# Kernel optimization log

Hardware: AMD Instinct MI355X
Metric: run time of the kernel (lower is better)

Reference implementation:

```python
import jax, jax.numpy as jnp
import numpy as np

NEG_INF = -1e10
DIST_THRESH = 0


def _collect_entities(rep, pos, mask):
    # rep: [B, N, H]; pos: [B, M, S] int; mask: [B, M, S] float
    B, M, S = pos.shape
    g = jnp.take_along_axis(rep, pos.reshape(B, M * S)[:, :, None], axis=1)  # [B, M*S, H]
    g = g.reshape(B, M, S, rep.shape[-1]) * mask[..., None]
    return g.sum(axis=2)  # [B, M, H]


def setup_inputs() -> dict:
    key = jax.random.key(0)
    ks = jax.random.split(key, 10)
    B, N, H = 8, 2048, 512
    M, S = 96, 16
    E, D, R, MAXD = 256, 64, 5, 600
    scale = 0.02
    return {
        'node_hidden': jax.random.normal(ks[0], (B, N, H), jnp.float32),
        'chem_map': jax.random.randint(ks[1], (B, M, S), 0, N),
        'chem_mask': jnp.ones((B, M, S), jnp.float32),
        'dis_map': jax.random.randint(ks[2], (B, M, S), 0, N),
        'dis_mask': jnp.ones((B, M, S), jnp.float32),
        'distance': jax.random.randint(ks[3], (B, M, M), 0, MAXD),
        'W_chem': jax.random.normal(ks[4], (H, E), jnp.float32) * scale,
        'b_chem': jnp.zeros((E,), jnp.float32),
        'W_dis': jax.random.normal(ks[5], (H, E), jnp.float32) * scale,
        'b_dis': jnp.zeros((E,), jnp.float32),
        'W_score': jax.random.normal(ks[6], (2 * E + H + D, R), jnp.float32) * scale,
        'b_score': jnp.zeros((R,), jnp.float32),
        'dist_emb': jax.random.normal(ks[7], (MAXD, D), jnp.float32) * scale,
    }


def reference(node_hidden, chem_map, chem_mask, dis_map, dis_mask, distance,
              W_chem, b_chem, W_dis, b_dis, W_score, b_score, dist_emb):
    B, M = chem_map.shape[0], chem_map.shape[1]
    E = W_chem.shape[1]

    # sentence representation: max-pool over tokens  -> [B, H]
    sent = jnp.max(node_hidden, axis=1)

    # gather mention spans, masked sum pool, tanh-linear  -> [B, M, E]
    chem = jnp.tanh(_collect_entities(node_hidden, chem_map, chem_mask) @ W_chem + b_chem)
    dis = jnp.tanh(_collect_entities(node_hidden, dis_map, dis_mask) @ W_dis + b_dis)

    dist_e = dist_emb[distance]  # [B, M, M, D]

    # pairwise concat: [chem_i, dis_j, dist_ij, sent]  -> [B, M, M, 2E+D+H]
    concat = jnp.concatenate([
        jnp.broadcast_to(chem[:, :, None, :], (B, M, M, E)),
        jnp.broadcast_to(dis[:, None, :, :], (B, M, M, E)),
        dist_e,
        jnp.broadcast_to(sent[:, None, None, :], (B, M, M, sent.shape[-1])),
    ], axis=-1)

    score = jnp.einsum('bmnf,fr->bmnr', concat, W_score) + b_score  # [B, M, M, R]

    # validity masks: non-empty spans and distance >= threshold
    chem_valid = chem_mask.sum(axis=-1) > 0  # [B, M]
    dis_valid = dis_mask.sum(axis=-1) > 0    # [B, M]
    pair_valid = chem_valid[:, :, None] & dis_valid[:, None, :]  # [B, M, M]
    valid = pair_valid & (distance >= DIST_THRESH)
    score = jnp.where(valid[..., None], score, NEG_INF)

    # max-pool over all mention pairs  -> [B, R]
    return jnp.max(score.reshape(B, M * M, -1), axis=1)
```

## Files before the change

### kernel.cpp

```cpp
#include <hip/hip_runtime.h>
#include <math.h>

constexpr int B = 8, N = 2048, H = 512, M = 96, S = 16;
constexpr int E = 256, D = 64, R = 5, MAXD = 600;
constexpr int NZ = 64;
constexpr int NCHUNK = N / NZ;
constexpr int MT = 8;
constexpr int HC = 4;
constexpr int HCHUNK = H / HC;
constexpr float NEG_INF = -1e10f;

constexpr int K1_SENT = 256;
constexpr int K1_POOL = 2 * B * M;
constexpr int K2_GEMM = (M / MT) * B * 2 * HC;
constexpr int K2_SENT = B;
constexpr int K2_DIST = MAXD / 4;

__device__ inline void atomicMaxFloat(float* addr, float val) {
    int* ai = (int*)addr;
    int old = *ai;
    while (__int_as_float(old) < val) {
        int assumed = old;
        old = atomicCAS(ai, assumed, __float_as_int(val));
        if (old == assumed) break;
    }
}

__global__ void k1(const float* __restrict__ node,
                   const int* __restrict__ cmap, const float* __restrict__ cmask,
                   const int* __restrict__ dmap, const float* __restrict__ dmask,
                   float* __restrict__ part, float* __restrict__ pooled,
                   float* __restrict__ validAB) {
    int blk = blockIdx.x, t = threadIdx.x;
    __shared__ int   smap[S];
    __shared__ float smask[S];

    if (blk < K1_SENT) {
        int b = blk >> 5;
        int z = ((blk & 31) << 1) + (t >> 7);
        int tt = t & 127;
        const float4* p = reinterpret_cast<const float4*>(
            node + ((size_t)b * N + (size_t)z * NCHUNK) * H) + tt;
        float4 mx = p[0];
        #pragma unroll
        for (int n = 1; n < NCHUNK; ++n) {
            float4 v = p[(size_t)n * (H / 4)];
            mx.x = fmaxf(mx.x, v.x); mx.y = fmaxf(mx.y, v.y);
            mx.z = fmaxf(mx.z, v.z); mx.w = fmaxf(mx.w, v.w);
        }
        reinterpret_cast<float4*>(part + ((size_t)z * B + b) * H)[tt] = mx;
    } else {
        int j = blk - K1_SENT;
        int m = j % M, b = (j / M) % B, z = j / (M * B);
        const int*   map  = z ? dmap  : cmap;
        const float* mask = z ? dmask : cmask;
        if (t < S) {
            size_t off = ((size_t)b * M + m) * S + t;
            smap[t]  = map[off];
            smask[t] = mask[off];
        }
        __syncthreads();
        float a0 = 0.f, a1 = 0.f;
        #pragma unroll
        for (int s = 0; s < S; ++s) {
            float mk = smask[s];
            const float2 v = reinterpret_cast<const float2*>(
                node + ((size_t)b * N + smap[s]) * H)[t];
            a0 += mk * v.x; a1 += mk * v.y;
        }
        size_t row = ((size_t)z * B + b) * M + m;
        reinterpret_cast<float2*>(pooled + row * H)[t] = make_float2(a0, a1);
        if (t == 0) {
            float ms = 0.f;
            #pragma unroll
            for (int s = 0; s < S; ++s) ms += smask[s];
            validAB[row] = (ms > 0.f) ? 1.f : 0.f;
        }
    }
}

__global__ void k2(const float* __restrict__ pooled,
                   const float* __restrict__ Wc, const float* __restrict__ Wd,
                   const float* __restrict__ part, const float* __restrict__ Wsc,
                   const float* __restrict__ bsc, const float* __restrict__ emb,
                   float* __restrict__ dotp, float* __restrict__ sS,
                   float* __restrict__ sD, float* __restrict__ out) {
    int blk = blockIdx.x, t = threadIdx.x;
    __shared__ float lp[MT][HCHUNK];
    __shared__ float sent[H];
    __shared__ float red[R][4];

    if (blk < K2_GEMM) {
        int mg  = blk % (M / MT);
        int b   = (blk / (M / MT)) % B;
        int zhc = blk / ((M / MT) * B);
        int z = zhc >> 2, hc = zhc & 3;
        const float* W = z ? Wd : Wc;

        for (int i = t; i < MT * HCHUNK; i += 256) {
            int mi = i >> 7, hh = i & (HCHUNK - 1);
            lp[mi][hh] = pooled[(((size_t)z * B + b) * M + mg * MT + mi) * H + hc * HCHUNK + hh];
        }
        __syncthreads();

        float acc[MT] = {};
        const float* Wp = W + (size_t)(hc * HCHUNK) * E + t;
        for (int hh = 0; hh < HCHUNK; hh += 4) {
            float w0 = Wp[(size_t)(hh + 0) * E];
            float w1 = Wp[(size_t)(hh + 1) * E];
            float w2 = Wp[(size_t)(hh + 2) * E];
            float w3 = Wp[(size_t)(hh + 3) * E];
            #pragma unroll
            for (int mi = 0; mi < MT; ++mi) {
                const float4 pv = *reinterpret_cast<const float4*>(&lp[mi][hh]);
                acc[mi] += pv.x * w0 + pv.y * w1 + pv.z * w2 + pv.w * w3;
            }
        }
        #pragma unroll
        for (int mi = 0; mi < MT; ++mi) {
            size_t row = ((size_t)z * B + b) * M + mg * MT + mi;
            dotp[((size_t)hc * (2 * B * M) + row) * E + t] = acc[mi];
        }
    } else if (blk < K2_GEMM + K2_SENT) {
        int b = blk - K2_GEMM;
        if (b == 0 && t < B * R) out[t] = NEG_INF;
        for (int h = t; h < H; h += 256) {
            float mx = -INFINITY;
            for (int z = 0; z < NZ; ++z) mx = fmaxf(mx, part[((size_t)z * B + b) * H + h]);
            sent[h] = mx;
        }
        __syncthreads();
        float acc[R] = {};
        for (int h = t; h < H; h += 256) {
            float v = sent[h];
            const float* w = Wsc + (size_t)(2 * E + D + h) * R;
            #pragma unroll
            for (int r = 0; r < R; ++r) acc[r] += v * w[r];
        }
        int wave = t >> 6, lane = t & 63;
        #pragma unroll
        for (int r = 0; r < R; ++r) {
            float v = acc[r];
            for (int off = 32; off; off >>= 1) v += __shfl_down(v, off, 64);
            if (lane == 0) red[r][wave] = v;
        }
        __syncthreads();
        if (t < R) sS[b * R + t] = red[t][0] + red[t][1] + red[t][2] + red[t][3] + bsc[t];
    } else {
        int d = (blk - K2_GEMM - K2_SENT) * 4 + (t >> 6);
        int k = t & 63;
        float v = emb[(size_t)d * D + k];
        #pragma unroll
        for (int r = 0; r < R; ++r) {
            float p = v * Wsc[(size_t)(2 * E + k) * R + r];
            for (int off = 32; off; off >>= 1) p += __shfl_down(p, off, 64);
            if (k == 0) sD[d * R + r] = p;
        }
    }
}

__global__ void k3(const float* __restrict__ dotp,
                   const float* __restrict__ bc, const float* __restrict__ bd,
                   const float* __restrict__ Wsc, const float* __restrict__ sS,
                   float* __restrict__ sAB) {
    int rid = blockIdx.x * 4 + (threadIdx.x >> 6);
    int lane = threadIdx.x & 63;
    int z = rid / (B * M);
    int b = (rid % (B * M)) / M;
    const float* bias = z ? bd : bc;
    int scoff = z ? E : 0;

    float4 dv = make_float4(0.f, 0.f, 0.f, 0.f);
    #pragma unroll
    for (int hc = 0; hc < HC; ++hc) {
        float4 v = reinterpret_cast<const float4*>(dotp + ((size_t)hc * (2 * B * M) + rid) * E)[lane];
        dv.x += v.x; dv.y += v.y; dv.z += v.z; dv.w += v.w;
    }
    float4 bv = reinterpret_cast<const float4*>(bias)[lane];
    float v0 = tanhf(dv.x + bv.x);
    float v1 = tanhf(dv.y + bv.y);
    float v2 = tanhf(dv.z + bv.z);
    float v3 = tanhf(dv.w + bv.w);

    int e0 = scoff + lane * 4;
    float p[R];
    #pragma unroll
    for (int r = 0; r < R; ++r) {
        p[r] = v0 * Wsc[(size_t)(e0 + 0) * R + r] + v1 * Wsc[(size_t)(e0 + 1) * R + r]
             + v2 * Wsc[(size_t)(e0 + 2) * R + r] + v3 * Wsc[(size_t)(e0 + 3) * R + r];
    }
    #pragma unroll
    for (int r = 0; r < R; ++r) {
        for (int off = 32; off; off >>= 1) p[r] += __shfl_down(p[r], off, 64);
    }
    if (lane == 0) {
        #pragma unroll
        for (int r = 0; r < R; ++r) {
            float add = (z == 0) ? sS[b * R + r] : 0.f;
            sAB[(size_t)rid * R + r] = p[r] + add;
        }
    }
}

__global__ void k4(const int* __restrict__ distance,
                   const float* __restrict__ sAB, const float* __restrict__ validAB,
                   const float* __restrict__ sD, float* __restrict__ out) {
    int g = blockIdx.x, b = blockIdx.y;
    int t = threadIdx.x;
    __shared__ float lB[M * R];
    __shared__ float lD[MAXD * R];
    __shared__ float lA[MT * R];
    __shared__ float lvA[MT], lvB[M];
    __shared__ float red[R][4];

    for (int i = t; i < M * R; i += 256) lB[i] = sAB[((size_t)(B + b)) * M * R + i];
    for (int i = t; i < MAXD * R; i += 256) lD[i] = sD[i];
    if (t < MT * R) lA[t] = sAB[((size_t)b * M + g * MT) * R + t];
    if (t < MT) lvA[t] = validAB[(size_t)b * M + g * MT + t];
    for (int i = t; i < M; i += 256) lvB[i] = validAB[((size_t)B + b) * M + i];
    __syncthreads();

    float mx[R];
    #pragma unroll
    for (int r = 0; r < R; ++r) mx[r] = NEG_INF;

    #pragma unroll
    for (int it = 0; it < (MT * M) / 256; ++it) {
        int idx = it * 256 + t;
        int mi = idx / M, n = idx % M;
        int dist = distance[((size_t)b * M + g * MT + mi) * M + n];
        if (lvA[mi] > 0.f && lvB[n] > 0.f && dist >= 0 ) {
            #pragma unroll
            for (int r = 0; r < R; ++r)
                mx[r] = fmaxf(mx[r], lA[mi * R + r] + lB[n * R + r] + lD[dist * R + r]);
        }
    }
    int wave = t >> 6, lane = t & 63;
    #pragma unroll
    for (int r = 0; r < R; ++r) {
        float v = mx[r];
        for (int off = 32; off; off >>= 1) v = fmaxf(v, __shfl_down(v, off, 64));
        if (lane == 0) red[r][wave] = v;
    }
    __syncthreads();
    if (t < R) {
        float v = fmaxf(fmaxf(red[t][0], red[t][1]), fmaxf(red[t][2], red[t][3]));
        atomicMaxFloat(out + b * R + t, v);
    }
}

extern "C" void kernel_launch(void* const* d_in, const int* in_sizes, int n_in,
                              void* d_out, int out_size, void* d_ws, size_t ws_size,
                              hipStream_t stream) {
    const float* node     = (const float*)d_in[0];
    const int*   cmap     = (const int*)  d_in[1];
    const float* cmask    = (const float*)d_in[2];
    const int*   dmap     = (const int*)  d_in[3];
    const float* dmask    = (const float*)d_in[4];
    const int*   distance = (const int*)  d_in[5];
    const float* Wc       = (const float*)d_in[6];
    const float* bc       = (const float*)d_in[7];
    const float* Wd       = (const float*)d_in[8];
    const float* bd       = (const float*)d_in[9];
    const float* Wsc      = (const float*)d_in[10];
    const float* bsc      = (const float*)d_in[11];
    const float* emb      = (const float*)d_in[12];
    float* out = (float*)d_out;

    float* ws      = (float*)d_ws;
    float* part    = ws;
    float* sS      = part + (size_t)NZ * B * H;
    float* sAB     = sS + B * R;
    float* validAB = sAB + 2 * B * M * R;
    float* sD      = validAB + 2 * B * M;
    float* pooled  = sD + MAXD * R;
    float* dotp    = pooled + (size_t)2 * B * M * H;

    hipLaunchKernelGGL(k1, dim3(K1_SENT + K1_POOL), dim3(256), 0, stream,
                       node, cmap, cmask, dmap, dmask, part, pooled, validAB);
    hipLaunchKernelGGL(k2, dim3(K2_GEMM + K2_SENT + K2_DIST), dim3(256), 0, stream,
                       pooled, Wc, Wd, part, Wsc, bsc, emb, dotp, sS, sD, out);
    hipLaunchKernelGGL(k3, dim3(2 * B * M / 4), dim3(256), 0, stream,
                       dotp, bc, bd, Wsc, sS, sAB);
    hipLaunchKernelGGL(k4, dim3(M / MT, B), dim3(256), 0, stream,
                       distance, sAB, validAB, sD, out);
}
```

Measured before the change: 61.34 us.

## Fuse four kernels into one cooperative persistent kernel with grid syncs

Replaces the four-launch pipeline with a single cooperative kernel that runs three phases separated by grid.sync. The GEMM stage now covers the full hidden dimension per block and fuses bias, tanh and the score projection in place, which removes the dotp partials and the separate k3 pass. The aim is to cut launch gaps and intermediate global traffic. In exchange it adds grid-wide barrier cost, and fewer GEMM blocks each do longer serial work. The old multi-kernel path is kept as a fallback if the cooperative launch fails.

```diff
diff --git a/kernel.cpp b/kernel.cpp
--- a/kernel.cpp
+++ b/kernel.cpp
@@ -1,20 +1,25 @@
 #include <hip/hip_runtime.h>
+#include <hip/hip_cooperative_groups.h>
 #include <math.h>
+
+namespace cg = cooperative_groups;
 
 constexpr int B = 8, N = 2048, H = 512, M = 96, S = 16;
 constexpr int E = 256, D = 64, R = 5, MAXD = 600;
 constexpr int NZ = 64;
 constexpr int NCHUNK = N / NZ;
-constexpr int MT = 8;
+constexpr int MT2 = 4;
+constexpr int MT  = 8;
 constexpr int HC = 4;
 constexpr int HCHUNK = H / HC;
+constexpr int MT4 = 8;
 constexpr float NEG_INF = -1e10f;
 
-constexpr int K1_SENT = 256;
-constexpr int K1_POOL = 2 * B * M;
-constexpr int K2_GEMM = (M / MT) * B * 2 * HC;
-constexpr int K2_SENT = B;
-constexpr int K2_DIST = MAXD / 4;
+constexpr int P1_SENT  = 256;
+constexpr int P1_ITEMS = P1_SENT + 2 * B * M;
+constexpr int NGEMM    = (M / MT2) * B * 2;
+constexpr int P2_ITEMS = NGEMM + B + MAXD / 4;
+constexpr int P3_ITEMS = (M / MT4) * B;
 
 __device__ inline void atomicMaxFloat(float* addr, float val) {
     int* ai = (int*)addr;
@@ -25,6 +30,225 @@
         if (old == assumed) break;
     }
 }
+
+__global__ __launch_bounds__(256, 4)
+void k_all(const float* __restrict__ node,
+           const int* __restrict__ cmap, const float* __restrict__ cmask,
+           const int* __restrict__ dmap, const float* __restrict__ dmask,
+           const int* __restrict__ distance,
+           const float* __restrict__ Wc, const float* __restrict__ bc,
+           const float* __restrict__ Wd, const float* __restrict__ bd,
+           const float* __restrict__ Wsc, const float* __restrict__ bsc,
+           const float* __restrict__ emb,
+           float* __restrict__ part, float* __restrict__ pooled,
+           float* __restrict__ validAB, float* __restrict__ sS,
+           float* __restrict__ sAB, float* __restrict__ sD,
+           float* __restrict__ out) {
+    cg::grid_group grid = cg::this_grid();
+    const int t = threadIdx.x;
+    const int blk = blockIdx.x;
+    const int GD = gridDim.x;
+
+    __shared__ float4 lp4[MT2][H / 4];
+    __shared__ int    smap[S];
+    __shared__ float  smask[S];
+    __shared__ float  sent[H];
+    __shared__ float  red2[4][MT2 * R];
+    __shared__ float  red[R][4];
+    __shared__ float  lB[M * R];
+    __shared__ float  lD[MAXD * R];
+    __shared__ float  lA[MT4 * R];
+    __shared__ float  lvA[MT4], lvB[M];
+
+    for (int item = blk; item < P1_ITEMS; item += GD) {
+        if (item < P1_SENT) {
+            int b = item >> 5;
+            int z = ((item & 31) << 1) + (t >> 7);
+            int tt = t & 127;
+            const float4* p = reinterpret_cast<const float4*>(
+                node + ((size_t)b * N + (size_t)z * NCHUNK) * H) + tt;
+            float4 mx = p[0];
+            #pragma unroll
+            for (int n = 1; n < NCHUNK; ++n) {
+                float4 v = p[(size_t)n * (H / 4)];
+                mx.x = fmaxf(mx.x, v.x); mx.y = fmaxf(mx.y, v.y);
+                mx.z = fmaxf(mx.z, v.z); mx.w = fmaxf(mx.w, v.w);
+            }
+            reinterpret_cast<float4*>(part + ((size_t)z * B + b) * H)[tt] = mx;
+        } else {
+            int j = item - P1_SENT;
+            int m = j % M, b = (j / M) % B, z = j / (M * B);
+            const int*   map  = z ? dmap  : cmap;
+            const float* mask = z ? dmask : cmask;
+            __syncthreads();
+            if (t < S) {
+                size_t off = ((size_t)b * M + m) * S + t;
+                smap[t]  = map[off];
+                smask[t] = mask[off];
+            }
+            __syncthreads();
+            float a0 = 0.f, a1 = 0.f;
+            #pragma unroll
+            for (int s = 0; s < S; ++s) {
+                float mk = smask[s];
+                const float2 v = reinterpret_cast<const float2*>(
+                    node + ((size_t)b * N + smap[s]) * H)[t];
+                a0 += mk * v.x; a1 += mk * v.y;
+            }
+            size_t row = ((size_t)z * B + b) * M + m;
+            reinterpret_cast<float2*>(pooled + row * H)[t] = make_float2(a0, a1);
+            if (t == 0) {
+                float ms = 0.f;
+                #pragma unroll
+                for (int s = 0; s < S; ++s) ms += smask[s];
+                validAB[row] = (ms > 0.f) ? 1.f : 0.f;
+            }
+        }
+    }
+    if (blk == 0 && t < B * R) out[t] = NEG_INF;
+
+    grid.sync();
+
+    for (int item = blk; item < P2_ITEMS; item += GD) {
+        __syncthreads();
+        if (item < NGEMM) {
+            int mg = item % (M / MT2);
+            int b  = (item / (M / MT2)) % B;
+            int z  = item / ((M / MT2) * B);
+            const float* W    = z ? Wd : Wc;
+            const float* bias = z ? bd : bc;
+            int scoff = z ? E : 0;
+
+            for (int i = t; i < MT2 * (H / 4); i += 256) {
+                int mi = i >> 7, c4 = i & 127;
+                lp4[mi][c4] = reinterpret_cast<const float4*>(
+                    pooled + (((size_t)z * B + b) * M + mg * MT2 + mi) * H)[c4];
+            }
+            __syncthreads();
+
+            float acc[MT2] = {};
+            const float* Wp = W + t;
+            for (int h = 0; h < H; h += 4) {
+                float w0 = Wp[(size_t)(h + 0) * E];
+                float w1 = Wp[(size_t)(h + 1) * E];
+                float w2 = Wp[(size_t)(h + 2) * E];
+                float w3 = Wp[(size_t)(h + 3) * E];
+                #pragma unroll
+                for (int mi = 0; mi < MT2; ++mi) {
+                    const float4 pv = lp4[mi][h >> 2];
+                    acc[mi] += pv.x * w0 + pv.y * w1 + pv.z * w2 + pv.w * w3;
+                }
+            }
+            float be = bias[t];
+            float v[MT2];
+            #pragma unroll
+            for (int mi = 0; mi < MT2; ++mi) v[mi] = tanhf(acc[mi] + be);
+
+            float w5[R];
+            #pragma unroll
+            for (int r = 0; r < R; ++r) w5[r] = Wsc[(size_t)(scoff + t) * R + r];
+            int wave = t >> 6, lane = t & 63;
+            #pragma unroll
+            for (int mi = 0; mi < MT2; ++mi) {
+                #pragma unroll
+                for (int r = 0; r < R; ++r) {
+                    float p = v[mi] * w5[r];
+                    for (int off = 32; off; off >>= 1) p += __shfl_down(p, off, 64);
+                    if (lane == 0) red2[wave][mi * R + r] = p;
+                }
+            }
+            __syncthreads();
+            if (t < MT2 * R) {
+                float s = red2[0][t] + red2[1][t] + red2[2][t] + red2[3][t];
+                int mi = t / R, r = t % R;
+                sAB[(((size_t)z * B + b) * M + mg * MT2 + mi) * R + r] = s;
+            }
+        } else if (item < NGEMM + B) {
+            int b = item - NGEMM;
+            for (int h = t; h < H; h += 256) {
+                float mx = -INFINITY;
+                for (int z = 0; z < NZ; ++z) mx = fmaxf(mx, part[((size_t)z * B + b) * H + h]);
+                sent[h] = mx;
+            }
+            __syncthreads();
+            float acc[R] = {};
+            for (int h = t; h < H; h += 256) {
+                float v = sent[h];
+                const float* w = Wsc + (size_t)(2 * E + D + h) * R;
+                #pragma unroll
+                for (int r = 0; r < R; ++r) acc[r] += v * w[r];
+            }
+            int wave = t >> 6, lane = t & 63;
+            #pragma unroll
+            for (int r = 0; r < R; ++r) {
+                float v = acc[r];
+                for (int off = 32; off; off >>= 1) v += __shfl_down(v, off, 64);
+                if (lane == 0) red[r][wave] = v;
+            }
+            __syncthreads();
+            if (t < R) sS[b * R + t] = red[t][0] + red[t][1] + red[t][2] + red[t][3] + bsc[t];
+        } else {
+            int d = (item - NGEMM - B) * 4 + (t >> 6);
+            int k = t & 63;
+            float v = emb[(size_t)d * D + k];
+            #pragma unroll
+            for (int r = 0; r < R; ++r) {
+                float p = v * Wsc[(size_t)(2 * E + k) * R + r];
+                for (int off = 32; off; off >>= 1) p += __shfl_down(p, off, 64);
+                if (k == 0) sD[d * R + r] = p;
+            }
+        }
+    }
+
+    grid.sync();
+
+    for (int item = blk; item < P3_ITEMS; item += GD) {
+        int g = item % (M / MT4);
+        int b = item / (M / MT4);
+        __syncthreads();
+
+        for (int i = t; i < M * R; i += 256) lB[i] = sAB[((size_t)(B + b)) * M * R + i];
+        for (int i = t; i < MAXD * R; i += 256) lD[i] = sD[i];
+        if (t < MT4 * R) lA[t] = sAB[((size_t)b * M + g * MT4) * R + t] + sS[b * R + (t % R)];
+        if (t < MT4) lvA[t] = validAB[(size_t)b * M + g * MT4 + t];
+        for (int i = t; i < M; i += 256) lvB[i] = validAB[((size_t)B + b) * M + i];
+        __syncthreads();
+
+        float mx[R];
+        #pragma unroll
+        for (int r = 0; r < R; ++r) mx[r] = NEG_INF;
+
+        #pragma unroll
+        for (int it = 0; it < (MT4 * M) / 256; ++it) {
+            int idx = it * 256 + t;
+            int mi = idx / M, n = idx % M;
+            int dist = distance[((size_t)b * M + g * MT4 + mi) * M + n];
+            if (lvA[mi] > 0.f && lvB[n] > 0.f && dist >= 0 ) {
+                #pragma unroll
+                for (int r = 0; r < R; ++r)
+                    mx[r] = fmaxf(mx[r], lA[mi * R + r] + lB[n * R + r] + lD[dist * R + r]);
+            }
+        }
+        int wave = t >> 6, lane = t & 63;
+        #pragma unroll
+        for (int r = 0; r < R; ++r) {
+            float v = mx[r];
+            for (int off = 32; off; off >>= 1) v = fmaxf(v, __shfl_down(v, off, 64));
+            if (lane == 0) red[r][wave] = v;
+        }
+        __syncthreads();
+        if (t < R) {
+            float v = fmaxf(fmaxf(red[t][0], red[t][1]), fmaxf(red[t][2], red[t][3]));
+            atomicMaxFloat(out + b * R + t, v);
+        }
+    }
+}
+
+constexpr int K1_SENT = 256;
+constexpr int K1_POOL = 2 * B * M;
+constexpr int K2_GEMM = (M / MT) * B * 2 * HC;
+constexpr int K2_SENT = B;
+constexpr int K2_DIST = MAXD / 4;
 
 __global__ void k1(const float* __restrict__ node,
                    const int* __restrict__ cmap, const float* __restrict__ cmask,
@@ -34,7 +258,6 @@
     int blk = blockIdx.x, t = threadIdx.x;
     __shared__ int   smap[S];
     __shared__ float smask[S];
-
     if (blk < K1_SENT) {
         int b = blk >> 5;
         int z = ((blk & 31) << 1) + (t >> 7);
@@ -89,20 +312,17 @@
     __shared__ float lp[MT][HCHUNK];
     __shared__ float sent[H];
     __shared__ float red[R][4];
-
     if (blk < K2_GEMM) {
         int mg  = blk % (M / MT);
         int b   = (blk / (M / MT)) % B;
         int zhc = blk / ((M / MT) * B);
         int z = zhc >> 2, hc = zhc & 3;
         const float* W = z ? Wd : Wc;
-
         for (int i = t; i < MT * HCHUNK; i += 256) {
             int mi = i >> 7, hh = i & (HCHUNK - 1);
             lp[mi][hh] = pooled[(((size_t)z * B + b) * M + mg * MT + mi) * H + hc * HCHUNK + hh];
         }
         __syncthreads();
-
         float acc[MT] = {};
         const float* Wp = W + (size_t)(hc * HCHUNK) * E + t;
         for (int hh = 0; hh < HCHUNK; hh += 4) {
@@ -169,7 +389,6 @@
     int b = (rid % (B * M)) / M;
     const float* bias = z ? bd : bc;
     int scoff = z ? E : 0;
-
     float4 dv = make_float4(0.f, 0.f, 0.f, 0.f);
     #pragma unroll
     for (int hc = 0; hc < HC; ++hc) {
@@ -181,7 +400,6 @@
     float v1 = tanhf(dv.y + bv.y);
     float v2 = tanhf(dv.z + bv.z);
     float v3 = tanhf(dv.w + bv.w);
-
     int e0 = scoff + lane * 4;
     float p[R];
     #pragma unroll
@@ -209,27 +427,24 @@
     int t = threadIdx.x;
     __shared__ float lB[M * R];
     __shared__ float lD[MAXD * R];
-    __shared__ float lA[MT * R];
-    __shared__ float lvA[MT], lvB[M];
+    __shared__ float lA[MT4 * R];
+    __shared__ float lvA[MT4], lvB[M];
     __shared__ float red[R][4];
-
     for (int i = t; i < M * R; i += 256) lB[i] = sAB[((size_t)(B + b)) * M * R + i];
     for (int i = t; i < MAXD * R; i += 256) lD[i] = sD[i];
-    if (t < MT * R) lA[t] = sAB[((size_t)b * M + g * MT) * R + t];
-    if (t < MT) lvA[t] = validAB[(size_t)b * M + g * MT + t];
+    if (t < MT4 * R) lA[t] = sAB[((size_t)b * M + g * MT4) * R + t];
+    if (t < MT4) lvA[t] = validAB[(size_t)b * M + g * MT4 + t];
     for (int i = t; i < M; i += 256) lvB[i] = validAB[((size_t)B + b) * M + i];
     __syncthreads();
-
     float mx[R];
     #pragma unroll
     for (int r = 0; r < R; ++r) mx[r] = NEG_INF;
-
     #pragma unroll
-    for (int it = 0; it < (MT * M) / 256; ++it) {
+    for (int it = 0; it < (MT4 * M) / 256; ++it) {
         int idx = it * 256 + t;
         int mi = idx / M, n = idx % M;
-        int dist = distance[((size_t)b * M + g * MT + mi) * M + n];
-        if (lvA[mi] > 0.f && lvB[n] > 0.f && dist >= 0 ) {
+        int dist = distance[((size_t)b * M + g * MT4 + mi) * M + n];
+        if (lvA[mi] > 0.f && lvB[n] > 0.f && dist >= 0) {
             #pragma unroll
             for (int r = 0; r < R; ++r)
                 mx[r] = fmaxf(mx[r], lA[mi * R + r] + lB[n * R + r] + lD[dist * R + r]);
@@ -276,12 +491,30 @@
     float* pooled  = sD + MAXD * R;
     float* dotp    = pooled + (size_t)2 * B * M * H;
 
-    hipLaunchKernelGGL(k1, dim3(K1_SENT + K1_POOL), dim3(256), 0, stream,
-                       node, cmap, cmask, dmap, dmask, part, pooled, validAB);
-    hipLaunchKernelGGL(k2, dim3(K2_GEMM + K2_SENT + K2_DIST), dim3(256), 0, stream,
-                       pooled, Wc, Wd, part, Wsc, bsc, emb, dotp, sS, sD, out);
-    hipLaunchKernelGGL(k3, dim3(2 * B * M / 4), dim3(256), 0, stream,
-                       dotp, bc, bd, Wsc, sS, sAB);
-    hipLaunchKernelGGL(k4, dim3(M / MT, B), dim3(256), 0, stream,
-                       distance, sAB, validAB, sD, out);
-}
+    int occ = 0;
+    hipError_t qerr = hipOccupancyMaxActiveBlocksPerMultiprocessor(&occ, k_all, 256, 0);
+    int grid = occ * 256;
+    if (grid > 1024) grid = 1024;
+
+    hipError_t lerr = hipErrorUnknown;
+    if (qerr == hipSuccess && grid >= 64) {
+        void* args[] = {
+            (void*)&node, (void*)&cmap, (void*)&cmask, (void*)&dmap, (void*)&dmask,
+            (void*)&distance, (void*)&Wc, (void*)&bc, (void*)&Wd, (void*)&bd,
+            (void*)&Wsc, (void*)&bsc, (void*)&emb,
+            (void*)&part, (void*)&pooled, (void*)&validAB, (void*)&sS,
+            (void*)&sAB, (void*)&sD, (void*)&out
+        };
+        lerr = hipLaunchCooperativeKernel((void*)k_all, dim3(grid), dim3(256), args, 0, stream);
+    }
+    if (lerr != hipSuccess) {
+        hipLaunchKernelGGL(k1, dim3(K1_SENT + K1_POOL), dim3(256), 0, stream,
+                           node, cmap, cmask, dmap, dmask, part, pooled, validAB);
+        hipLaunchKernelGGL(k2, dim3(K2_GEMM + K2_SENT + K2_DIST), dim3(256), 0, stream,
+                           pooled, Wc, Wd, part, Wsc, bsc, emb, dotp, sS, sD, out);
+        hipLaunchKernelGGL(k3, dim3(2 * B * M / 4), dim3(256), 0, stream,
+                           dotp, bc, bd, Wsc, sS, sAB);
+        hipLaunchKernelGGL(k4, dim3(M / MT4, B), dim3(256), 0, stream,
+                           distance, sAB, validAB, sD, out);
+    }
+}
```

New measurement: 183.4 us. 199% more time.

## Fuse four kernels into two, computing span pooling and projection in one block

Applied to the files above, without the earlier changes.

Merges the gather-pool, projection GEMM, tanh and score-reduction stages into one kernel in which each block pools four mentions into shared memory and immediately multiplies them by the full H×E weight. The per-batch sentence score is moved into the final max kernel. This removes two launches and the global round trips through the pooled and split-K dotp buffers. In exchange, each GEMM block now walks the full H=512 reduction serially with only 4 rows per weight load, so weight reuse drops. Every final block also recomputes the sentence max over 64 partials.

```diff
diff --git a/kernel.cpp b/kernel.cpp
--- a/kernel.cpp
+++ b/kernel.cpp
@@ -5,16 +5,14 @@
 constexpr int E = 256, D = 64, R = 5, MAXD = 600;
 constexpr int NZ = 64;
 constexpr int NCHUNK = N / NZ;
-constexpr int MT = 8;
-constexpr int HC = 4;
-constexpr int HCHUNK = H / HC;
+constexpr int MTA = 4;
+constexpr int MT4 = 8;
 constexpr float NEG_INF = -1e10f;
 
-constexpr int K1_SENT = 256;
-constexpr int K1_POOL = 2 * B * M;
-constexpr int K2_GEMM = (M / MT) * B * 2 * HC;
-constexpr int K2_SENT = B;
-constexpr int K2_DIST = MAXD / 4;
+constexpr int A_SENT = 256;
+constexpr int A_GEMM = 2 * B * (M / MTA);
+constexpr int A_DIST = MAXD / 4;
+constexpr int A_GRID = A_SENT + A_GEMM + A_DIST;
 
 __device__ inline void atomicMaxFloat(float* addr, float val) {
     int* ai = (int*)addr;
@@ -26,16 +24,21 @@
     }
 }
 
-__global__ void k1(const float* __restrict__ node,
+__global__ void kA(const float* __restrict__ node,
                    const int* __restrict__ cmap, const float* __restrict__ cmask,
                    const int* __restrict__ dmap, const float* __restrict__ dmask,
-                   float* __restrict__ part, float* __restrict__ pooled,
-                   float* __restrict__ validAB) {
-    int blk = blockIdx.x, t = threadIdx.x;
-    __shared__ int   smap[S];
-    __shared__ float smask[S];
-
-    if (blk < K1_SENT) {
+                   const float* __restrict__ Wc, const float* __restrict__ bc,
+                   const float* __restrict__ Wd, const float* __restrict__ bd,
+                   const float* __restrict__ Wsc, const float* __restrict__ emb,
+                   float* __restrict__ part, float* __restrict__ sAB,
+                   float* __restrict__ validAB, float* __restrict__ sD,
+                   float* __restrict__ out) {
+    const int blk = blockIdx.x;
+    const int t = threadIdx.x;
+
+    if (blk == 0 && t < B * R) out[t] = NEG_INF;
+
+    if (blk < A_SENT) {
         int b = blk >> 5;
         int z = ((blk & 31) << 1) + (t >> 7);
         int tt = t & 127;
@@ -49,105 +52,85 @@
             mx.z = fmaxf(mx.z, v.z); mx.w = fmaxf(mx.w, v.w);
         }
         reinterpret_cast<float4*>(part + ((size_t)z * B + b) * H)[tt] = mx;
-    } else {
-        int j = blk - K1_SENT;
-        int m = j % M, b = (j / M) % B, z = j / (M * B);
+    } else if (blk < A_SENT + A_GEMM) {
+        int j  = blk - A_SENT;
+        int mg = j % (M / MTA);
+        int b  = (j / (M / MTA)) % B;
+        int z  = j / ((M / MTA) * B);
+        const float* W    = z ? Wd : Wc;
+        const float* bias = z ? bd : bc;
         const int*   map  = z ? dmap  : cmap;
         const float* mask = z ? dmask : cmask;
-        if (t < S) {
-            size_t off = ((size_t)b * M + m) * S + t;
-            smap[t]  = map[off];
-            smask[t] = mask[off];
+        int scoff = z ? E : 0;
+
+        __shared__ float pooled[MTA][H];
+        __shared__ int   smap[MTA][S];
+        __shared__ float smask[MTA][S];
+
+        if (t < MTA * S) {
+            int mi = t >> 4, s = t & 15;
+            size_t off = ((size_t)b * M + mg * MTA + mi) * S + s;
+            smap[mi][s]  = map[off];
+            smask[mi][s] = mask[off];
         }
         __syncthreads();
-        float a0 = 0.f, a1 = 0.f;
-        #pragma unroll
-        for (int s = 0; s < S; ++s) {
-            float mk = smask[s];
-            const float2 v = reinterpret_cast<const float2*>(
-                node + ((size_t)b * N + smap[s]) * H)[t];
-            a0 += mk * v.x; a1 += mk * v.y;
-        }
-        size_t row = ((size_t)z * B + b) * M + m;
-        reinterpret_cast<float2*>(pooled + row * H)[t] = make_float2(a0, a1);
-        if (t == 0) {
+
+        #pragma unroll
+        for (int mi = 0; mi < MTA; ++mi) {
+            float a0 = 0.f, a1 = 0.f;
+            #pragma unroll
+            for (int s = 0; s < S; ++s) {
+                float mk = smask[mi][s];
+                const float2 v = reinterpret_cast<const float2*>(
+                    node + ((size_t)b * N + smap[mi][s]) * H)[t];
+                a0 += mk * v.x; a1 += mk * v.y;
+            }
+            reinterpret_cast<float2*>(&pooled[mi][0])[t] = make_float2(a0, a1);
+        }
+        if (t < MTA) {
             float ms = 0.f;
             #pragma unroll
-            for (int s = 0; s < S; ++s) ms += smask[s];
-            validAB[row] = (ms > 0.f) ? 1.f : 0.f;
-        }
-    }
-}
-
-__global__ void k2(const float* __restrict__ pooled,
-                   const float* __restrict__ Wc, const float* __restrict__ Wd,
-                   const float* __restrict__ part, const float* __restrict__ Wsc,
-                   const float* __restrict__ bsc, const float* __restrict__ emb,
-                   float* __restrict__ dotp, float* __restrict__ sS,
-                   float* __restrict__ sD, float* __restrict__ out) {
-    int blk = blockIdx.x, t = threadIdx.x;
-    __shared__ float lp[MT][HCHUNK];
-    __shared__ float sent[H];
-    __shared__ float red[R][4];
-
-    if (blk < K2_GEMM) {
-        int mg  = blk % (M / MT);
-        int b   = (blk / (M / MT)) % B;
-        int zhc = blk / ((M / MT) * B);
-        int z = zhc >> 2, hc = zhc & 3;
-        const float* W = z ? Wd : Wc;
-
-        for (int i = t; i < MT * HCHUNK; i += 256) {
-            int mi = i >> 7, hh = i & (HCHUNK - 1);
-            lp[mi][hh] = pooled[(((size_t)z * B + b) * M + mg * MT + mi) * H + hc * HCHUNK + hh];
+            for (int s = 0; s < S; ++s) ms += smask[t][s];
+            validAB[((size_t)z * B + b) * M + mg * MTA + t] = (ms > 0.f) ? 1.f : 0.f;
         }
         __syncthreads();
 
-        float acc[MT] = {};
-        const float* Wp = W + (size_t)(hc * HCHUNK) * E + t;
-        for (int hh = 0; hh < HCHUNK; hh += 4) {
-            float w0 = Wp[(size_t)(hh + 0) * E];
-            float w1 = Wp[(size_t)(hh + 1) * E];
-            float w2 = Wp[(size_t)(hh + 2) * E];
-            float w3 = Wp[(size_t)(hh + 3) * E];
-            #pragma unroll
-            for (int mi = 0; mi < MT; ++mi) {
-                const float4 pv = *reinterpret_cast<const float4*>(&lp[mi][hh]);
-                acc[mi] += pv.x * w0 + pv.y * w1 + pv.z * w2 + pv.w * w3;
-            }
-        }
-        #pragma unroll
-        for (int mi = 0; mi < MT; ++mi) {
-            size_t row = ((size_t)z * B + b) * M + mg * MT + mi;
-            dotp[((size_t)hc * (2 * B * M) + row) * E + t] = acc[mi];
-        }
-    } else if (blk < K2_GEMM + K2_SENT) {
-        int b = blk - K2_GEMM;
-        if (b == 0 && t < B * R) out[t] = NEG_INF;
-        for (int h = t; h < H; h += 256) {
-            float mx = -INFINITY;
-            for (int z = 0; z < NZ; ++z) mx = fmaxf(mx, part[((size_t)z * B + b) * H + h]);
-            sent[h] = mx;
-        }
-        __syncthreads();
-        float acc[R] = {};
-        for (int h = t; h < H; h += 256) {
-            float v = sent[h];
-            const float* w = Wsc + (size_t)(2 * E + D + h) * R;
-            #pragma unroll
-            for (int r = 0; r < R; ++r) acc[r] += v * w[r];
-        }
-        int wave = t >> 6, lane = t & 63;
+        int eq = t & 63;
+        int mi = t >> 6;
+        const float4* W4 = reinterpret_cast<const float4*>(W) + eq;
+        const float* pm = &pooled[mi][0];
+        float4 acc = make_float4(0.f, 0.f, 0.f, 0.f);
+        #pragma unroll 8
+        for (int h = 0; h < H; ++h) {
+            float4 wv = W4[(size_t)h * (E / 4)];
+            float p = pm[h];
+            acc.x += p * wv.x; acc.y += p * wv.y;
+            acc.z += p * wv.z; acc.w += p * wv.w;
+        }
+        float4 bv = reinterpret_cast<const float4*>(bias)[eq];
+        float v0 = tanhf(acc.x + bv.x);
+        float v1 = tanhf(acc.y + bv.y);
+        float v2 = tanhf(acc.z + bv.z);
+        float v3 = tanhf(acc.w + bv.w);
+
+        int e0 = scoff + 4 * eq;
+        float p[R];
         #pragma unroll
         for (int r = 0; r < R; ++r) {
-            float v = acc[r];
-            for (int off = 32; off; off >>= 1) v += __shfl_down(v, off, 64);
-            if (lane == 0) red[r][wave] = v;
-        }
-        __syncthreads();
-        if (t < R) sS[b * R + t] = red[t][0] + red[t][1] + red[t][2] + red[t][3] + bsc[t];
+            p[r] = v0 * Wsc[(size_t)(e0 + 0) * R + r] + v1 * Wsc[(size_t)(e0 + 1) * R + r]
+                 + v2 * Wsc[(size_t)(e0 + 2) * R + r] + v3 * Wsc[(size_t)(e0 + 3) * R + r];
+        }
+        #pragma unroll
+        for (int r = 0; r < R; ++r) {
+            for (int off = 32; off; off >>= 1) p[r] += __shfl_down(p[r], off, 64);
+        }
+        if (eq == 0) {
+            size_t row = ((size_t)z * B + b) * M + mg * MTA + mi;
+            #pragma unroll
+            for (int r = 0; r < R; ++r) sAB[row * R + r] = p[r];
+        }
     } else {
-        int d = (blk - K2_GEMM - K2_SENT) * 4 + (t >> 6);
+        int d = (blk - A_SENT - A_GEMM) * 4 + (t >> 6);
         int k = t & 63;
         float v = emb[(size_t)d * D + k];
         #pragma unroll
@@ -159,64 +142,53 @@
     }
 }
 
-__global__ void k3(const float* __restrict__ dotp,
-                   const float* __restrict__ bc, const float* __restrict__ bd,
-                   const float* __restrict__ Wsc, const float* __restrict__ sS,
-                   float* __restrict__ sAB) {
-    int rid = blockIdx.x * 4 + (threadIdx.x >> 6);
-    int lane = threadIdx.x & 63;
-    int z = rid / (B * M);
-    int b = (rid % (B * M)) / M;
-    const float* bias = z ? bd : bc;
-    int scoff = z ? E : 0;
-
-    float4 dv = make_float4(0.f, 0.f, 0.f, 0.f);
-    #pragma unroll
-    for (int hc = 0; hc < HC; ++hc) {
-        float4 v = reinterpret_cast<const float4*>(dotp + ((size_t)hc * (2 * B * M) + rid) * E)[lane];
-        dv.x += v.x; dv.y += v.y; dv.z += v.z; dv.w += v.w;
-    }
-    float4 bv = reinterpret_cast<const float4*>(bias)[lane];
-    float v0 = tanhf(dv.x + bv.x);
-    float v1 = tanhf(dv.y + bv.y);
-    float v2 = tanhf(dv.z + bv.z);
-    float v3 = tanhf(dv.w + bv.w);
-
-    int e0 = scoff + lane * 4;
-    float p[R];
-    #pragma unroll
-    for (int r = 0; r < R; ++r) {
-        p[r] = v0 * Wsc[(size_t)(e0 + 0) * R + r] + v1 * Wsc[(size_t)(e0 + 1) * R + r]
-             + v2 * Wsc[(size_t)(e0 + 2) * R + r] + v3 * Wsc[(size_t)(e0 + 3) * R + r];
-    }
-    #pragma unroll
-    for (int r = 0; r < R; ++r) {
-        for (int off = 32; off; off >>= 1) p[r] += __shfl_down(p[r], off, 64);
-    }
-    if (lane == 0) {
-        #pragma unroll
-        for (int r = 0; r < R; ++r) {
-            float add = (z == 0) ? sS[b * R + r] : 0.f;
-            sAB[(size_t)rid * R + r] = p[r] + add;
-        }
-    }
-}
-
-__global__ void k4(const int* __restrict__ distance,
+__global__ void kB(const float* __restrict__ part, const float* __restrict__ Wsc,
+                   const float* __restrict__ bsc,
+                   const int* __restrict__ distance,
                    const float* __restrict__ sAB, const float* __restrict__ validAB,
                    const float* __restrict__ sD, float* __restrict__ out) {
-    int g = blockIdx.x, b = blockIdx.y;
-    int t = threadIdx.x;
+    const int g = blockIdx.x % (M / MT4);
+    const int b = blockIdx.x / (M / MT4);
+    const int t = threadIdx.x;
+
+    __shared__ float sent[H];
+    __shared__ float red[R][4];
+    __shared__ float sSb[R];
     __shared__ float lB[M * R];
     __shared__ float lD[MAXD * R];
-    __shared__ float lA[MT * R];
-    __shared__ float lvA[MT], lvB[M];
-    __shared__ float red[R][4];
+    __shared__ float lA[MT4 * R];
+    __shared__ float lvA[MT4], lvB[M];
+
+    for (int h = t; h < H; h += 256) {
+        float mx = -INFINITY;
+        #pragma unroll 8
+        for (int z = 0; z < NZ; ++z) mx = fmaxf(mx, part[((size_t)z * B + b) * H + h]);
+        sent[h] = mx;
+    }
+    __syncthreads();
+
+    float acc[R] = {};
+    for (int h = t; h < H; h += 256) {
+        float v = sent[h];
+        const float* w = Wsc + (size_t)(2 * E + D + h) * R;
+        #pragma unroll
+        for (int r = 0; r < R; ++r) acc[r] += v * w[r];
+    }
+    int wave = t >> 6, lane = t & 63;
+    #pragma unroll
+    for (int r = 0; r < R; ++r) {
+        float v = acc[r];
+        for (int off = 32; off; off >>= 1) v += __shfl_down(v, off, 64);
+        if (lane == 0) red[r][wave] = v;
+    }
+    __syncthreads();
+    if (t < R) sSb[t] = red[t][0] + red[t][1] + red[t][2] + red[t][3] + bsc[t];
+    __syncthreads();
 
     for (int i = t; i < M * R; i += 256) lB[i] = sAB[((size_t)(B + b)) * M * R + i];
     for (int i = t; i < MAXD * R; i += 256) lD[i] = sD[i];
-    if (t < MT * R) lA[t] = sAB[((size_t)b * M + g * MT) * R + t];
-    if (t < MT) lvA[t] = validAB[(size_t)b * M + g * MT + t];
+    if (t < MT4 * R) lA[t] = sAB[((size_t)b * M + g * MT4) * R + t] + sSb[t % R];
+    if (t < MT4) lvA[t] = validAB[(size_t)b * M + g * MT4 + t];
     for (int i = t; i < M; i += 256) lvB[i] = validAB[((size_t)B + b) * M + i];
     __syncthreads();
 
@@ -225,17 +197,16 @@
     for (int r = 0; r < R; ++r) mx[r] = NEG_INF;
 
     #pragma unroll
-    for (int it = 0; it < (MT * M) / 256; ++it) {
+    for (int it = 0; it < (MT4 * M) / 256; ++it) {
         int idx = it * 256 + t;
         int mi = idx / M, n = idx % M;
-        int dist = distance[((size_t)b * M + g * MT + mi) * M + n];
+        int dist = distance[((size_t)b * M + g * MT4 + mi) * M + n];
         if (lvA[mi] > 0.f && lvB[n] > 0.f && dist >= 0 ) {
             #pragma unroll
             for (int r = 0; r < R; ++r)
                 mx[r] = fmaxf(mx[r], lA[mi * R + r] + lB[n * R + r] + lD[dist * R + r]);
         }
     }
-    int wave = t >> 6, lane = t & 63;
     #pragma unroll
     for (int r = 0; r < R; ++r) {
         float v = mx[r];
@@ -269,19 +240,13 @@
 
     float* ws      = (float*)d_ws;
     float* part    = ws;
-    float* sS      = part + (size_t)NZ * B * H;
-    float* sAB     = sS + B * R;
+    float* sAB     = part + (size_t)NZ * B * H;
     float* validAB = sAB + 2 * B * M * R;
     float* sD      = validAB + 2 * B * M;
-    float* pooled  = sD + MAXD * R;
-    float* dotp    = pooled + (size_t)2 * B * M * H;
-
-    hipLaunchKernelGGL(k1, dim3(K1_SENT + K1_POOL), dim3(256), 0, stream,
-                       node, cmap, cmask, dmap, dmask, part, pooled, validAB);
-    hipLaunchKernelGGL(k2, dim3(K2_GEMM + K2_SENT + K2_DIST), dim3(256), 0, stream,
-                       pooled, Wc, Wd, part, Wsc, bsc, emb, dotp, sS, sD, out);
-    hipLaunchKernelGGL(k3, dim3(2 * B * M / 4), dim3(256), 0, stream,
-                       dotp, bc, bd, Wsc, sS, sAB);
-    hipLaunchKernelGGL(k4, dim3(M / MT, B), dim3(256), 0, stream,
-                       distance, sAB, validAB, sD, out);
-}
+
+    hipLaunchKernelGGL(kA, dim3(A_GRID), dim3(256), 0, stream,
+                       node, cmap, cmask, dmap, dmask, Wc, bc, Wd, bd, Wsc, emb,
+                       part, sAB, validAB, sD, out);
+    hipLaunchKernelGGL(kB, dim3((M / MT4) * B), dim3(256), 0, stream,
+                       part, Wsc, bsc, distance, sAB, validAB, sD, out);
+}
```

Result: slower. 79.80 us (+30.1%).
